# Optimization experiments

Measured on AMD Instinct MI355X. Metric: run time of the kernel, lower is better.

Reference implementation:

```python
import jax, jax.numpy as jnp
import numpy as np

B, T, D = 8, 1024, 1024

def setup_inputs() -> dict:
    key = jax.random.key(0)
    ks = jax.random.split(key, 9)
    s = D ** -0.5
    return {
        "x": jax.random.normal(ks[0], (B, T, D), dtype=jnp.float32),
        "w_q": jax.random.normal(ks[1], (D, D), dtype=jnp.float32) * s,
        "b_q": jax.random.normal(ks[2], (D,), dtype=jnp.float32) * 0.02,
        "w_k": jax.random.normal(ks[3], (D, D), dtype=jnp.float32) * s,
        "b_k": jax.random.normal(ks[4], (D,), dtype=jnp.float32) * 0.02,
        "w_v": jax.random.normal(ks[5], (D, D), dtype=jnp.float32) * s,
        "b_v": jax.random.normal(ks[6], (D,), dtype=jnp.float32) * 0.02,
        "w_o": jax.random.normal(ks[7], (D, D), dtype=jnp.float32) * s,
        "b_o": jax.random.normal(ks[8], (D,), dtype=jnp.float32) * 0.02,
    }

def reference(x, w_q, b_q, w_k, b_k, w_v, b_v, w_o, b_o):
    d = x.shape[-1]
    scale = jnp.asarray(d, x.dtype) ** -0.5
    q = jnp.einsum('btd,ed->bte', x, w_q) + b_q  # nn.Linear: x @ W^T + b
    k = jnp.einsum('btd,ed->bte', x, w_k) + b_k
    v = jnp.einsum('btd,ed->bte', x, w_v) + b_v
    t = x.shape[1]
    causal = jnp.tril(jnp.ones((t, t), dtype=bool))  # (T, T)
    scores = jnp.einsum('bqd,bkd->bqk', q, k) * scale
    scores = jnp.where(causal, scores, -jnp.inf)
    attn = jax.nn.softmax(scores, axis=-1)  # max-subtraction folded in
    out = jnp.einsum('bqk,bkd->bqd', attn, v)
    return jnp.einsum('btd,ed->bte', out, w_o) + b_o
```

## Files before the change

kernel.cpp:

```cpp
#include <hip/hip_runtime.h>

typedef unsigned short u16;
typedef __attribute__((ext_vector_type(8))) short short8;
typedef __attribute__((ext_vector_type(4))) float f32x4;


__device__ __forceinline__ u16 f2bf(float f) {
  unsigned u = __builtin_bit_cast(unsigned, f);
  u += 0x7fffu + ((u >> 16) & 1u);
  return (u16)(u >> 16);
}

__device__ __forceinline__ void gload16(const void* g, void* l) {
  __builtin_amdgcn_global_load_lds(
      (const __attribute__((address_space(1))) unsigned*)g,
      (__attribute__((address_space(3))) unsigned*)l, 16, 0, 0);
}

__device__ __forceinline__ void gemm_tile(
    const u16* __restrict__ A, int lda,
    const u16* __restrict__ B, int ldb,
    int m0, int n0, int kend,
    char* sA, char* sB, f32x4 acc[4][4])
{
  const int tid  = threadIdx.x;
  const int lane = tid & 63;
  const int wave = tid >> 6;
  const int quad = lane >> 4;
  const int l16  = lane & 15;
  const int wr   = (wave >> 1) << 6;
  const int wc   = (wave & 1) << 6;

  const u16* ga[4]; const u16* gb[4]; int lb[4];
#pragma unroll
  for (int j = 0; j < 4; ++j) {
    const int Lb = j * 256 + wave * 64;
    const int L  = Lb + lane;
    const int r  = L >> 3;
    const int c  = (L & 7) ^ (r & 7);
    lb[j] = Lb * 16;
    ga[j] = A + (size_t)(m0 + r) * lda + c * 8;
    gb[j] = B + (size_t)(n0 + r) * ldb + c * 8;
  }

  for (int kt = 0; kt < kend; kt += 64) {
#pragma unroll
    for (int j = 0; j < 4; ++j) {
      gload16(ga[j], sA + lb[j]);
      gload16(gb[j], sB + lb[j]);
      ga[j] += 64; gb[j] += 64;
    }
    __syncthreads();
#pragma unroll
    for (int kk = 0; kk < 2; ++kk) {
      short8 af[4], bfr[4];
#pragma unroll
      for (int i = 0; i < 4; ++i) {
        const int rm = wr + i * 16 + l16;
        af[i]  = *(const short8*)(sA + rm * 128 + (((kk << 2) + quad) ^ (rm & 7)) * 16);
        const int rn = wc + i * 16 + l16;
        bfr[i] = *(const short8*)(sB + rn * 128 + (((kk << 2) + quad) ^ (rn & 7)) * 16);
      }
#pragma unroll
      for (int i = 0; i < 4; ++i)
#pragma unroll
        for (int j = 0; j < 4; ++j)
          acc[i][j] = __builtin_amdgcn_mfma_f32_16x16x32_bf16(af[i], bfr[j], acc[i][j], 0, 0, 0);
    }
    __syncthreads();
  }
}

#define ACC_ZERO(acc) { const f32x4 z4 = {0.f,0.f,0.f,0.f}; \
  _Pragma("unroll") for (int i=0;i<4;++i) _Pragma("unroll") for (int j=0;j<4;++j) acc[i][j]=z4; }

__device__ __forceinline__ void store_tile_bf16(
    f32x4 acc[4][4], const float* bias, int nbias0,
    u16* C, int m0, int n0, int ldc, char* smem)
{
  const int tid = threadIdx.x, lane = tid & 63, wave = tid >> 6;
  const int quad = lane >> 4, l16 = lane & 15;
  const int wr = (wave >> 1) << 6, wc = (wave & 1) << 6;
  u16* t = (u16*)smem;
#pragma unroll
  for (int j = 0; j < 4; ++j) {
    const int nn = wc + j * 16 + l16;
    const float bj = bias ? bias[nbias0 + nn] : 0.f;
#pragma unroll
    for (int i = 0; i < 4; ++i) {
      const int mm = wr + i * 16 + quad * 4;
#pragma unroll
      for (int r = 0; r < 4; ++r)
        t[(mm + r) * 136 + nn] = f2bf(acc[i][j][r] + bj);
    }
  }
  __syncthreads();
#pragma unroll
  for (int it = 0; it < 8; ++it) {
    const int L = it * 256 + tid;
    const int mm = L >> 4, cc = L & 15;
    *(uint4*)(C + (size_t)(m0 + mm) * ldc + n0 + cc * 8) =
        *(const uint4*)(t + mm * 136 + cc * 8);
  }
}

__global__ __launch_bounds__(256) void cast_inputs(
    const float* __restrict__ x,  const float* __restrict__ wq,
    const float* __restrict__ wk, const float* __restrict__ wv,
    const float* __restrict__ wo,
    u16* xb, u16* wqb, u16* wkb, u16* wvb, u16* wob)
{
  int b = blockIdx.x;
  const float* src; u16* dst; int base;
  if (b < 4096) { src = x; dst = xb; base = b * 2048; }
  else {
    int r = (b - 4096) >> 9, bb = (b - 4096) & 511;
    base = bb * 2048;
    src = (r == 0) ? wq : (r == 1) ? wk : (r == 2) ? wv : wo;
    dst = (r == 0) ? wqb : (r == 1) ? wkb : (r == 2) ? wvb : wob;
  }
  int i0 = base + threadIdx.x * 8;
  float4 f0 = *(const float4*)(src + i0);
  float4 f1 = *(const float4*)(src + i0 + 4);
  short8 o;
  o[0]=(short)f2bf(f0.x); o[1]=(short)f2bf(f0.y); o[2]=(short)f2bf(f0.z); o[3]=(short)f2bf(f0.w);
  o[4]=(short)f2bf(f1.x); o[5]=(short)f2bf(f1.y); o[6]=(short)f2bf(f1.z); o[7]=(short)f2bf(f1.w);
  *(short8*)(dst + i0) = o;
}

__global__ __launch_bounds__(256) void proj_qkv(
    const u16* __restrict__ xb,
    const u16* __restrict__ wqb, const u16* __restrict__ wkb, const u16* __restrict__ wvb,
    const float* __restrict__ bq, const float* __restrict__ bk, const float* __restrict__ bv,
    u16* q, u16* k, u16* vt)
{
  __shared__ char smem[34816];
  char* sA = smem; char* sB = smem + 16384;
  const int z = blockIdx.z;
  const u16* W = (z == 0) ? wqb : (z == 1) ? wkb : wvb;
  const float* bias = (z == 0) ? bq : (z == 1) ? bk : bv;
  const int id = blockIdx.x + 8 * blockIdx.y;
  const int m0 = ((id & 7) * 8 + (id >> 6)) * 128;
  const int n0 = ((id >> 3) & 7) * 128;

  f32x4 acc[4][4]; ACC_ZERO(acc);
  gemm_tile(xb, 1024, W, 1024, m0, n0, 1024, sA, sB, acc);

  if (z < 2) {
    store_tile_bf16(acc, bias, n0, (z == 0) ? q : k, m0, n0, 1024, smem);
  } else {
    const int tid = threadIdx.x, lane = tid & 63, wave = tid >> 6;
    const int quad = lane >> 4, l16 = lane & 15;
    const int wr = (wave >> 1) << 6, wc = (wave & 1) << 6;
    u16* t = (u16*)smem;
#pragma unroll
    for (int j = 0; j < 4; ++j) {
      const int nn = wc + j * 16 + l16;
      const float bj = bias[n0 + nn];
#pragma unroll
      for (int i = 0; i < 4; ++i) {
        const int mm = wr + i * 16 + quad * 4;
#pragma unroll
        for (int r = 0; r < 4; ++r)
          t[nn * 136 + mm + r] = f2bf(acc[i][j][r] + bj);
      }
    }
    __syncthreads();
    const int b = m0 >> 10, t0 = m0 & 1023;
#pragma unroll
    for (int it = 0; it < 8; ++it) {
      const int L = it * 256 + tid;
      const int nn = L >> 4, cc = L & 15;
      *(uint4*)(vt + ((size_t)b << 20) + (size_t)(n0 + nn) * 1024 + t0 + cc * 8) =
          *(const uint4*)(t + nn * 136 + cc * 8);
    }
  }
}

__global__ __launch_bounds__(256) void qk_scores(
    const u16* __restrict__ q, const u16* __restrict__ k, float* __restrict__ sc)
{
  const int kb = blockIdx.x, qb = blockIdx.y, b = blockIdx.z;
  if (kb > qb) return;
  __shared__ char smem[32768];
  const u16* A = q + ((size_t)b << 20);
  const u16* B = k + ((size_t)b << 20);
  float* C = sc + ((size_t)b << 20);
  const int m0 = qb * 128, n0 = kb * 128;

  f32x4 acc[4][4]; ACC_ZERO(acc);
  gemm_tile(A, 1024, B, 1024, m0, n0, 1024, smem, smem + 16384, acc);

  const int tid = threadIdx.x, lane = tid & 63, wave = tid >> 6;
  const int quad = lane >> 4, l16 = lane & 15;
  const int wr = (wave >> 1) << 6, wc = (wave & 1) << 6;
#pragma unroll
  for (int j = 0; j < 4; ++j) {
    const int n = n0 + wc + j * 16 + l16;
#pragma unroll
    for (int i = 0; i < 4; ++i) {
      const int m = m0 + wr + i * 16 + quad * 4;
#pragma unroll
      for (int r = 0; r < 4; ++r)
        C[(size_t)(m + r) * 1024 + n] = acc[i][j][r] * 0.03125f;
    }
  }
}

__global__ __launch_bounds__(256) void softmax_causal(float* __restrict__ sc)
{
  const int row = blockIdx.x;
  const int qi = row & 1023;
  float* s = sc + (size_t)row * 1024;
  const int tid = threadIdx.x, lane = tid & 63, wave = tid >> 6;
  __shared__ float red[4];

  float v[4]; float mx = -1e30f;
#pragma unroll
  for (int it = 0; it < 4; ++it) {
    const int k2 = tid + it * 256;
    v[it] = (k2 <= qi) ? s[k2] : -1e30f;
    mx = fmaxf(mx, v[it]);
  }
  for (int o = 32; o; o >>= 1) mx = fmaxf(mx, __shfl_down(mx, o));
  if (lane == 0) red[wave] = mx;
  __syncthreads();
  mx = fmaxf(fmaxf(red[0], red[1]), fmaxf(red[2], red[3]));
  __syncthreads();

  float e[4]; float sum = 0.f;
#pragma unroll
  for (int it = 0; it < 4; ++it) {
    const int k2 = tid + it * 256;
    e[it] = (k2 <= qi) ? __expf(v[it] - mx) : 0.f;
    sum += e[it];
  }
  for (int o = 32; o; o >>= 1) sum += __shfl_down(sum, o);
  if (lane == 0) red[wave] = sum;
  __syncthreads();
  sum = red[0] + red[1] + red[2] + red[3];
  const float inv = 1.f / sum;

  u16* p = (u16*)s;
#pragma unroll
  for (int it = 0; it < 4; ++it)
    p[tid + it * 256] = f2bf(e[it] * inv);
}

__global__ __launch_bounds__(256) void pv_gemm(
    const float* __restrict__ sc, const u16* __restrict__ vt, u16* __restrict__ o)
{
  const int nb = blockIdx.x, qb = blockIdx.y, b = blockIdx.z;
  __shared__ char smem[34816];
  const u16* A = (const u16*)(sc + ((size_t)b << 20));
  const u16* B = vt + ((size_t)b << 20);
  const int m0 = qb * 128, n0 = nb * 128;
  const int kend = (qb + 1) * 128;

  f32x4 acc[4][4]; ACC_ZERO(acc);
  gemm_tile(A, 2048, B, 1024, m0, n0, kend, smem, smem + 16384, acc);

  store_tile_bf16(acc, nullptr, 0, o + ((size_t)b << 20), m0, n0, 1024, smem);
}

__global__ __launch_bounds__(256) void proj_o(
    const u16* __restrict__ ob, const u16* __restrict__ wob,
    const float* __restrict__ bo, float* __restrict__ out)
{
  __shared__ char smem[32768];
  const int id = blockIdx.x + 8 * blockIdx.y;
  const int m0 = ((id & 7) * 8 + (id >> 6)) * 128;
  const int n0 = ((id >> 3) & 7) * 128;
  f32x4 acc[4][4]; ACC_ZERO(acc);
  gemm_tile(ob, 1024, wob, 1024, m0, n0, 1024, smem, smem + 16384, acc);

  const int tid = threadIdx.x, lane = tid & 63, wave = tid >> 6;
  const int quad = lane >> 4, l16 = lane & 15;
  const int wr = (wave >> 1) << 6, wc = (wave & 1) << 6;
#pragma unroll
  for (int j = 0; j < 4; ++j) {
    const int n = n0 + wc + j * 16 + l16;
    const float bj = bo[n];
#pragma unroll
    for (int i = 0; i < 4; ++i) {
      const int m = m0 + wr + i * 16 + quad * 4;
#pragma unroll
      for (int r = 0; r < 4; ++r)
        out[(size_t)(m + r) * 1024 + n] = acc[i][j][r] + bj;
    }
  }
}

extern "C" void kernel_launch(void* const* d_in, const int* in_sizes, int n_in,
                              void* d_out, int out_size, void* d_ws, size_t ws_size,
                              hipStream_t stream) {
  const float* x  = (const float*)d_in[0];
  const float* wq = (const float*)d_in[1];
  const float* bq = (const float*)d_in[2];
  const float* wk = (const float*)d_in[3];
  const float* bk = (const float*)d_in[4];
  const float* wv = (const float*)d_in[5];
  const float* bv = (const float*)d_in[6];
  const float* wo = (const float*)d_in[7];
  const float* bo = (const float*)d_in[8];
  float* out = (float*)d_out;

  char* ws = (char*)d_ws;
  const size_t MB = 1u << 20;
  u16*  xb  = (u16*)(ws);
  u16*  wqb = (u16*)(ws + 16*MB);
  u16*  wkb = (u16*)(ws + 18*MB);
  u16*  wvb = (u16*)(ws + 20*MB);
  u16*  wob = (u16*)(ws + 22*MB);
  u16*  qb  = (u16*)(ws + 24*MB);
  u16*  kb  = (u16*)(ws + 40*MB);
  u16*  vtb = (u16*)(ws + 56*MB);
  float* sc = (float*)(ws + 72*MB);

  cast_inputs<<<6144, 256, 0, stream>>>(x, wq, wk, wv, wo, xb, wqb, wkb, wvb, wob);
  proj_qkv<<<dim3(8, 64, 3), 256, 0, stream>>>(xb, wqb, wkb, wvb, bq, bk, bv, qb, kb, vtb);
  qk_scores<<<dim3(8, 8, 8), 256, 0, stream>>>(qb, kb, sc);
  softmax_causal<<<8192, 256, 0, stream>>>(sc);
  pv_gemm<<<dim3(8, 8, 8), 256, 0, stream>>>(sc, vtb, xb );
  proj_o<<<dim3(8, 64), 256, 0, stream>>>(xb, wob, bo, out);
}
```

Baseline: 241.7 us.

## Fuse softmax exp into QK scores kernel and defer normalization to PV

```diff
diff --git a/kernel.cpp b/kernel.cpp
--- a/kernel.cpp
+++ b/kernel.cpp
@@ -177,15 +177,19 @@
   }
 }
 
-__global__ __launch_bounds__(256) void qk_scores(
-    const u16* __restrict__ q, const u16* __restrict__ k, float* __restrict__ sc)
-{
-  const int kb = blockIdx.x, qb = blockIdx.y, b = blockIdx.z;
-  if (kb > qb) return;
-  __shared__ char smem[32768];
+__global__ __launch_bounds__(256) void qk_expscores(
+    const u16* __restrict__ q, const u16* __restrict__ k,
+    u16* __restrict__ probs, float* __restrict__ rowsum)
+{
+  const int id = blockIdx.x;
+  const int b = id / 36, t = id - b * 36;
+  const int qb = (t >= 28) ? 7 : (t >= 21) ? 6 : (t >= 15) ? 5 : (t >= 10) ? 4
+               : (t >= 6) ? 3 : (t >= 3) ? 2 : (t >= 1) ? 1 : 0;
+  const int kb = t - qb * (qb + 1) / 2;
+
+  __shared__ char smem[34816];
   const u16* A = q + ((size_t)b << 20);
   const u16* B = k + ((size_t)b << 20);
-  float* C = sc + ((size_t)b << 20);
   const int m0 = qb * 128, n0 = kb * 128;
 
   f32x4 acc[4][4]; ACC_ZERO(acc);
@@ -194,81 +198,98 @@
   const int tid = threadIdx.x, lane = tid & 63, wave = tid >> 6;
   const int quad = lane >> 4, l16 = lane & 15;
   const int wr = (wave >> 1) << 6, wc = (wave & 1) << 6;
+  const bool diag = (kb == qb);
+
+  float part[4][4];
+#pragma unroll
+  for (int i = 0; i < 4; ++i)
+#pragma unroll
+    for (int r = 0; r < 4; ++r) part[i][r] = 0.f;
+
+  u16* tl = (u16*)smem;
 #pragma unroll
   for (int j = 0; j < 4; ++j) {
-    const int n = n0 + wc + j * 16 + l16;
+    const int nn = wc + j * 16 + l16;
 #pragma unroll
     for (int i = 0; i < 4; ++i) {
-      const int m = m0 + wr + i * 16 + quad * 4;
-#pragma unroll
-      for (int r = 0; r < 4; ++r)
-        C[(size_t)(m + r) * 1024 + n] = acc[i][j][r] * 0.03125f;
-    }
-  }
-}
-
-__global__ __launch_bounds__(256) void softmax_causal(float* __restrict__ sc)
-{
-  const int row = blockIdx.x;
-  const int qi = row & 1023;
-  float* s = sc + (size_t)row * 1024;
-  const int tid = threadIdx.x, lane = tid & 63, wave = tid >> 6;
-  __shared__ float red[4];
-
-  float v[4]; float mx = -1e30f;
-#pragma unroll
-  for (int it = 0; it < 4; ++it) {
-    const int k2 = tid + it * 256;
-    v[it] = (k2 <= qi) ? s[k2] : -1e30f;
-    mx = fmaxf(mx, v[it]);
-  }
-  for (int o = 32; o; o >>= 1) mx = fmaxf(mx, __shfl_down(mx, o));
-  if (lane == 0) red[wave] = mx;
+      const int mm = wr + i * 16 + quad * 4;
+#pragma unroll
+      for (int r = 0; r < 4; ++r) {
+        float e = __expf(acc[i][j][r] * 0.03125f);
+        if (diag && nn > mm + r) e = 0.f;
+        part[i][r] += e;
+        tl[(mm + r) * 136 + nn] = f2bf(e);
+      }
+    }
+  }
+  float* rs = rowsum + b * 1024 + m0;
+#pragma unroll
+  for (int i = 0; i < 4; ++i)
+#pragma unroll
+    for (int r = 0; r < 4; ++r) {
+      float v = part[i][r];
+      v += __shfl_xor(v, 1); v += __shfl_xor(v, 2);
+      v += __shfl_xor(v, 4); v += __shfl_xor(v, 8);
+      if (l16 == 0) atomicAdd(rs + wr + i * 16 + quad * 4 + r, v);
+    }
   __syncthreads();
-  mx = fmaxf(fmaxf(red[0], red[1]), fmaxf(red[2], red[3]));
-  __syncthreads();
-
-  float e[4]; float sum = 0.f;
-#pragma unroll
-  for (int it = 0; it < 4; ++it) {
-    const int k2 = tid + it * 256;
-    e[it] = (k2 <= qi) ? __expf(v[it] - mx) : 0.f;
-    sum += e[it];
-  }
-  for (int o = 32; o; o >>= 1) sum += __shfl_down(sum, o);
-  if (lane == 0) red[wave] = sum;
-  __syncthreads();
-  sum = red[0] + red[1] + red[2] + red[3];
-  const float inv = 1.f / sum;
-
-  u16* p = (u16*)s;
-#pragma unroll
-  for (int it = 0; it < 4; ++it)
-    p[tid + it * 256] = f2bf(e[it] * inv);
+  u16* C = probs + ((size_t)b << 20);
+#pragma unroll
+  for (int it = 0; it < 8; ++it) {
+    const int L = it * 256 + tid;
+    const int mm = L >> 4, cc = L & 15;
+    *(uint4*)(C + (size_t)(m0 + mm) * 1024 + n0 + cc * 8) =
+        *(const uint4*)(tl + mm * 136 + cc * 8);
+  }
 }
 
 __global__ __launch_bounds__(256) void pv_gemm(
-    const float* __restrict__ sc, const u16* __restrict__ vt, u16* __restrict__ o)
-{
-  const int nb = blockIdx.x, qb = blockIdx.y, b = blockIdx.z;
+    const u16* __restrict__ probs, const u16* __restrict__ vt,
+    const float* __restrict__ rowsum, u16* __restrict__ o)
+{
+  const int id = blockIdx.x;
+  const int b = id & 7, nb = (id >> 3) & 7, qb = 7 - (id >> 6);
   __shared__ char smem[34816];
-  const u16* A = (const u16*)(sc + ((size_t)b << 20));
+  const u16* A = probs + ((size_t)b << 20);
   const u16* B = vt + ((size_t)b << 20);
   const int m0 = qb * 128, n0 = nb * 128;
   const int kend = (qb + 1) * 128;
 
   f32x4 acc[4][4]; ACC_ZERO(acc);
-  gemm_tile(A, 2048, B, 1024, m0, n0, kend, smem, smem + 16384, acc);
-
-  store_tile_bf16(acc, nullptr, 0, o + ((size_t)b << 20), m0, n0, 1024, smem);
+  gemm_tile(A, 1024, B, 1024, m0, n0, kend, smem, smem + 16384, acc);
+
+  const int tid = threadIdx.x, lane = tid & 63, wave = tid >> 6;
+  const int quad = lane >> 4, l16 = lane & 15;
+  const int wr = (wave >> 1) << 6, wc = (wave & 1) << 6;
+  const float* rs = rowsum + b * 1024 + m0;
+  u16* tl = (u16*)smem;
+#pragma unroll
+  for (int i = 0; i < 4; ++i)
+#pragma unroll
+    for (int r = 0; r < 4; ++r) {
+      const int mm = wr + i * 16 + quad * 4 + r;
+      const float inv = 1.0f / rs[mm];
+#pragma unroll
+      for (int j = 0; j < 4; ++j)
+        tl[mm * 136 + wc + j * 16 + l16] = f2bf(acc[i][j][r] * inv);
+    }
+  __syncthreads();
+  u16* C = o + ((size_t)b << 20);
+#pragma unroll
+  for (int it = 0; it < 8; ++it) {
+    const int L = it * 256 + tid;
+    const int mm = L >> 4, cc = L & 15;
+    *(uint4*)(C + (size_t)(m0 + mm) * 1024 + n0 + cc * 8) =
+        *(const uint4*)(tl + mm * 136 + cc * 8);
+  }
 }
 
 __global__ __launch_bounds__(256) void proj_o(
     const u16* __restrict__ ob, const u16* __restrict__ wob,
     const float* __restrict__ bo, float* __restrict__ out)
 {
-  __shared__ char smem[32768];
-  const int id = blockIdx.x + 8 * blockIdx.y;
+  __shared__ char smem[34816];
+  const int id = blockIdx.x;
   const int m0 = ((id & 7) * 8 + (id >> 6)) * 128;
   const int n0 = ((id >> 3) & 7) * 128;
   f32x4 acc[4][4]; ACC_ZERO(acc);
@@ -277,17 +298,30 @@
   const int tid = threadIdx.x, lane = tid & 63, wave = tid >> 6;
   const int quad = lane >> 4, l16 = lane & 15;
   const int wr = (wave >> 1) << 6, wc = (wave & 1) << 6;
-#pragma unroll
-  for (int j = 0; j < 4; ++j) {
-    const int n = n0 + wc + j * 16 + l16;
-    const float bj = bo[n];
-#pragma unroll
-    for (int i = 0; i < 4; ++i) {
-      const int m = m0 + wr + i * 16 + quad * 4;
-#pragma unroll
-      for (int r = 0; r < 4; ++r)
-        out[(size_t)(m + r) * 1024 + n] = acc[i][j][r] + bj;
-    }
+  float* tf = (float*)smem;
+#pragma unroll
+  for (int half = 0; half < 2; ++half) {
+    if (wr == half * 64) {
+#pragma unroll
+      for (int j = 0; j < 4; ++j) {
+        const int nn = wc + j * 16 + l16;
+        const float bj = bo[n0 + nn];
+#pragma unroll
+        for (int i = 0; i < 4; ++i)
+#pragma unroll
+          for (int r = 0; r < 4; ++r)
+            tf[(i * 16 + quad * 4 + r) * 132 + nn] = acc[i][j][r] + bj;
+      }
+    }
+    __syncthreads();
+#pragma unroll
+    for (int it = 0; it < 8; ++it) {
+      const int L = it * 256 + tid;
+      const int mm = L >> 5, cc = L & 31;
+      *(float4*)(out + (size_t)(m0 + half * 64 + mm) * 1024 + n0 + cc * 4) =
+          *(const float4*)(tf + mm * 132 + cc * 4);
+    }
+    __syncthreads();
   }
 }
 
@@ -315,12 +349,13 @@
   u16*  qb  = (u16*)(ws + 24*MB);
   u16*  kb  = (u16*)(ws + 40*MB);
   u16*  vtb = (u16*)(ws + 56*MB);
-  float* sc = (float*)(ws + 72*MB);
+  u16*  pr  = (u16*)(ws + 72*MB);
+  float* rsum = (float*)(ws + 88*MB);
 
   cast_inputs<<<6144, 256, 0, stream>>>(x, wq, wk, wv, wo, xb, wqb, wkb, wvb, wob);
+  hipMemsetAsync(rsum, 0, 8192 * sizeof(float), stream);
   proj_qkv<<<dim3(8, 64, 3), 256, 0, stream>>>(xb, wqb, wkb, wvb, bq, bk, bv, qb, kb, vtb);
-  qk_scores<<<dim3(8, 8, 8), 256, 0, stream>>>(qb, kb, sc);
-  softmax_causal<<<8192, 256, 0, stream>>>(sc);
-  pv_gemm<<<dim3(8, 8, 8), 256, 0, stream>>>(sc, vtb, xb );
-  proj_o<<<dim3(8, 64), 256, 0, stream>>>(xb, wob, bo, out);
-}
+  qk_expscores<<<288, 256, 0, stream>>>(qb, kb, pr, rsum);
+  pv_gemm<<<512, 256, 0, stream>>>(pr, vtb, rsum, xb );
+  proj_o<<<512, 256, 0, stream>>>(xb, wob, bo, out);
+}
```

Result: faster. 236.3 us (-2.3%).
